# Kernel optimization log

Measured on AMD Instinct MI355X. Metric: run time of the kernel, lower is better.

Reference implementation:

```python
import jax, jax.numpy as jnp
import numpy as np

N_NODES = 100000
N_EDGES = 1600000
IN_NODE = 64
IN_EDGE = 16
HID = 128
OUT = 128
N_CONVS = 3
NEG_SLOPE = 0.01  # LeakyReLU default
LN_EPS = 1e-5


def setup_inputs() -> dict:
    key = jax.random.key(0)
    ks = jax.random.split(key, 16)
    x = jax.random.normal(ks[0], (N_NODES, IN_NODE), dtype=jnp.float32)
    edge_attr = jax.random.normal(ks[1], (N_EDGES, IN_EDGE), dtype=jnp.float32)
    edge_index = jax.random.randint(ks[2], (2, N_EDGES), 0, N_NODES, dtype=jnp.int64)
    # xavier-normal-ish init for linears
    def lin(k, fi, fo):
        return jax.random.normal(k, (fi, fo), dtype=jnp.float32) * jnp.sqrt(2.0 / (fi + fo))
    W_node = lin(ks[3], IN_NODE, HID)
    b_node = jnp.zeros((HID,), jnp.float32)
    W_edge = lin(ks[4], IN_EDGE, HID)
    b_edge = jnp.zeros((HID,), jnp.float32)
    W_conv = jax.random.normal(ks[5], (N_CONVS, HID, HID), dtype=jnp.float32) * jnp.sqrt(1.0 / HID)
    b_conv = jnp.zeros((N_CONVS, HID), jnp.float32)
    W_head = lin(ks[6], HID, OUT)
    b_head = jnp.zeros((OUT,), jnp.float32)
    ln_gamma = jnp.ones((OUT,), jnp.float32)
    ln_beta = jnp.zeros((OUT,), jnp.float32)
    return dict(x=x, edge_attr=edge_attr, edge_index=edge_index,
                W_node=W_node, b_node=b_node, W_edge=W_edge, b_edge=b_edge,
                W_conv=W_conv, b_conv=b_conv, W_head=W_head, b_head=b_head,
                ln_gamma=ln_gamma, ln_beta=ln_beta)


def _leaky_relu(x):
    return jnp.where(x >= 0, x, NEG_SLOPE * x)


def reference(x, edge_attr, edge_index, W_node, b_node, W_edge, b_edge,
              W_conv, b_conv, W_head, b_head, ln_gamma, ln_beta):
    src, dst = edge_index[0], edge_index[1]
    h = x @ W_node + b_node                  # [N, H]
    e = edge_attr @ W_edge + b_edge          # [E, H]
    skip = h
    for l in range(N_CONVS):
        # GINEConv (eps=0): nn((1+eps)*h_i + sum_j relu(h_j + e_ij)), nn = Linear + LeakyReLU
        msg = jax.nn.relu(h[src] + e)        # [E, H]
        agg = jax.ops.segment_sum(msg, dst, num_segments=N_NODES)  # [N, H]
        h = _leaky_relu((h + agg) @ W_conv[l] + b_conv[l])
    h = skip + h
    # head: Linear + LayerNorm
    y = h @ W_head + b_head                  # [N, OUT]
    mu = jnp.mean(y, axis=-1, keepdims=True)
    var = jnp.mean(jnp.square(y - mu), axis=-1, keepdims=True)
    return (y - mu) * jax.lax.rsqrt(var + LN_EPS) * ln_gamma + ln_beta
```

## Files before the change

### kernel.cpp

```cpp
#include <hip/hip_runtime.h>
#include <hip/hip_fp16.h>

constexpr int N      = 100000;
constexpr int E      = 1600000;
constexpr int F_IN   = 64;
constexpr int F_EDGE = 16;
constexpr int H      = 128;
constexpr int NB     = (N + 255) / 256;
constexpr float NEG  = 0.01f;
constexpr float EPS  = 1e-5f;

__global__ __launch_bounds__(256) void k_zero(int* __restrict__ p, int n) {
  int i = blockIdx.x * 256 + threadIdx.x;
  if (i < n) p[i] = 0;
}

__global__ __launch_bounds__(256) void k_hist(const int* __restrict__ eidx, int* __restrict__ deg) {
  int i = blockIdx.x * 256 + threadIdx.x;
  if (i < E) atomicAdd(&deg[eidx[E + i]], 1);
}

__global__ __launch_bounds__(256) void k_scan_block(const int* __restrict__ deg,
    int* __restrict__ excl, int* __restrict__ bsum) {
  __shared__ int s[256];
  int t = threadIdx.x, i = blockIdx.x * 256 + t;
  int v = (i < N) ? deg[i] : 0;
  s[t] = v; __syncthreads();
#pragma unroll
  for (int off = 1; off < 256; off <<= 1) {
    int u = (t >= off) ? s[t - off] : 0;
    __syncthreads();
    s[t] += u;
    __syncthreads();
  }
  if (i < N) excl[i] = s[t] - v;
  if (t == 255) bsum[blockIdx.x] = s[255];
}

__global__ __launch_bounds__(512) void k_scan_top(const int* __restrict__ bsum, int* __restrict__ boff) {
  __shared__ int s[512];
  int t = threadIdx.x;
  int v = (t < NB) ? bsum[t] : 0;
  s[t] = v; __syncthreads();
#pragma unroll
  for (int off = 1; off < 512; off <<= 1) {
    int u = (t >= off) ? s[t - off] : 0;
    __syncthreads();
    s[t] += u;
    __syncthreads();
  }
  if (t < NB) boff[t] = s[t] - v;
}

__global__ __launch_bounds__(256) void k_scan_add(const int* __restrict__ excl,
    const int* __restrict__ boff, int* __restrict__ rowptr, int* __restrict__ cursor) {
  int i = blockIdx.x * 256 + threadIdx.x;
  if (i < N) {
    int r = excl[i] + boff[i >> 8];
    rowptr[i] = r;
    cursor[i] = r;
  }
}

__global__ __launch_bounds__(256) void k_scatter(const int* __restrict__ eidx,
    const float* __restrict__ edge_attr, int* __restrict__ cursor,
    int* __restrict__ csr_src, uint4* __restrict__ csr_a16) {
  int i = blockIdx.x * 256 + threadIdx.x;
  if (i >= E) return;
  int d = eidx[E + i];
  int pos = atomicAdd(&cursor[d], 1);
  csr_src[pos] = eidx[i];
  const float4* ar = (const float4*)(edge_attr + (size_t)i * F_EDGE);
  float4 f0 = ar[0], f1 = ar[1], f2 = ar[2], f3 = ar[3];
  __half2 hh[8];
  hh[0] = __float22half2_rn(make_float2(f0.x, f0.y));
  hh[1] = __float22half2_rn(make_float2(f0.z, f0.w));
  hh[2] = __float22half2_rn(make_float2(f1.x, f1.y));
  hh[3] = __float22half2_rn(make_float2(f1.z, f1.w));
  hh[4] = __float22half2_rn(make_float2(f2.x, f2.y));
  hh[5] = __float22half2_rn(make_float2(f2.z, f2.w));
  hh[6] = __float22half2_rn(make_float2(f3.x, f3.y));
  hh[7] = __float22half2_rn(make_float2(f3.z, f3.w));
  const uint4* u = (const uint4*)hh;
  csr_a16[2 * (size_t)pos + 0] = u[0];
  csr_a16[2 * (size_t)pos + 1] = u[1];
}

__global__ __launch_bounds__(256) void k_node_linear(
    const float* __restrict__ x, const float* __restrict__ W,
    const float* __restrict__ b, float* __restrict__ h, __half* __restrict__ h16) {
  __shared__ float xs[8][F_IN];
  int i0 = blockIdx.x * 8;
  ((float2*)xs)[threadIdx.x] = ((const float2*)(x + (size_t)i0 * F_IN))[threadIdx.x];
  __syncthreads();
  int c = threadIdx.x & (H - 1);
  int j0 = (threadIdx.x >> 7) * 4;
  float bc = b[c];
  float acc[4] = {bc, bc, bc, bc};
#pragma unroll 8
  for (int k = 0; k < F_IN; ++k) {
    float wv = W[k * H + c];
#pragma unroll
    for (int j = 0; j < 4; ++j) acc[j] = fmaf(xs[j0 + j][k], wv, acc[j]);
  }
#pragma unroll
  for (int j = 0; j < 4; ++j) {
    size_t idx = (size_t)(i0 + j0 + j) * H + c;
    h[idx] = acc[j];
    h16[idx] = __float2half_rn(acc[j]);
  }
}

__device__ __forceinline__ float2 edge_mlp(uint4 a0, uint4 a1,
                                           const float2* __restrict__ w2, float2 t) {
  const __half2* pa = (const __half2*)&a0;
  const __half2* pb = (const __half2*)&a1;
#pragma unroll
  for (int j = 0; j < 4; ++j) {
    float2 f = __half22float2(pa[j]);
    t.x = fmaf(f.x, w2[2 * j].x, t.x);     t.y = fmaf(f.x, w2[2 * j].y, t.y);
    t.x = fmaf(f.y, w2[2 * j + 1].x, t.x); t.y = fmaf(f.y, w2[2 * j + 1].y, t.y);
  }
#pragma unroll
  for (int j = 0; j < 4; ++j) {
    float2 f = __half22float2(pb[j]);
    t.x = fmaf(f.x, w2[8 + 2 * j].x, t.x);     t.y = fmaf(f.x, w2[8 + 2 * j].y, t.y);
    t.x = fmaf(f.y, w2[8 + 2 * j + 1].x, t.x); t.y = fmaf(f.y, w2[8 + 2 * j + 1].y, t.y);
  }
  return t;
}

__global__ __launch_bounds__(256) void k_gather(
    const int* __restrict__ rowptr, const int* __restrict__ deg,
    const int* __restrict__ csr_src, const uint4* __restrict__ csr_a16,
    const __half2* __restrict__ h16, const float* __restrict__ We,
    const float* __restrict__ be, const float* __restrict__ h,
    float* __restrict__ sum) {
  int lane = threadIdx.x & 63;
  int node = (blockIdx.x * 256 + threadIdx.x) >> 6;
  if (node >= N) return;
  float2 w2[F_EDGE];
#pragma unroll
  for (int k = 0; k < F_EDGE; ++k) w2[k] = ((const float2*)(We + k * H))[lane];
  float2 bias = ((const float2*)be)[lane];
  float2 acc = ((const float2*)(h + (size_t)node * H))[lane];
  int p0 = rowptr[node];
  int pend = p0 + deg[node];
  int p = p0;
  for (; p + 2 <= pend; p += 2) {
    int s0 = csr_src[p];
    int s1 = csr_src[p + 1];
    __half2 g0 = h16[(size_t)s0 * 64 + lane];
    __half2 g1 = h16[(size_t)s1 * 64 + lane];
    uint4 a00 = csr_a16[2 * (size_t)p + 0];
    uint4 a01 = csr_a16[2 * (size_t)p + 1];
    uint4 a10 = csr_a16[2 * (size_t)p + 2];
    uint4 a11 = csr_a16[2 * (size_t)p + 3];
    float2 t0 = edge_mlp(a00, a01, w2, bias);
    float2 t1 = edge_mlp(a10, a11, w2, bias);
    float2 gf0 = __half22float2(g0);
    float2 gf1 = __half22float2(g1);
    acc.x += fmaxf(gf0.x + t0.x, 0.f) + fmaxf(gf1.x + t1.x, 0.f);
    acc.y += fmaxf(gf0.y + t0.y, 0.f) + fmaxf(gf1.y + t1.y, 0.f);
  }
  for (; p < pend; ++p) {
    int s = csr_src[p];
    __half2 g = h16[(size_t)s * 64 + lane];
    uint4 a0 = csr_a16[2 * (size_t)p + 0];
    uint4 a1 = csr_a16[2 * (size_t)p + 1];
    float2 t = edge_mlp(a0, a1, w2, bias);
    float2 gf = __half22float2(g);
    acc.x += fmaxf(gf.x + t.x, 0.f);
    acc.y += fmaxf(gf.y + t.y, 0.f);
  }
  ((float2*)sum)[(size_t)node * 64 + lane] = acc;
}

__global__ __launch_bounds__(256) void k_node_update(
    const float* __restrict__ sum, const float* __restrict__ W,
    const float* __restrict__ b, float* __restrict__ hout, __half* __restrict__ h16) {
  __shared__ float t[8][H];
  int i0 = blockIdx.x * 8;
  ((float4*)t)[threadIdx.x] = ((const float4*)(sum + (size_t)i0 * H))[threadIdx.x];
  __syncthreads();
  int c = threadIdx.x & (H - 1);
  int j0 = (threadIdx.x >> 7) * 4;
  float bc = b[c];
  float acc[4] = {bc, bc, bc, bc};
#pragma unroll 8
  for (int k = 0; k < H; ++k) {
    float wv = W[k * H + c];
#pragma unroll
    for (int j = 0; j < 4; ++j) acc[j] = fmaf(t[j0 + j][k], wv, acc[j]);
  }
#pragma unroll
  for (int j = 0; j < 4; ++j) {
    float a = acc[j];
    a = a >= 0.f ? a : NEG * a;
    size_t idx = (size_t)(i0 + j0 + j) * H + c;
    hout[idx] = a;
    h16[idx] = __float2half_rn(a);
  }
}

__global__ __launch_bounds__(128) void k_head(
    const float* __restrict__ x, const float* __restrict__ Wn,
    const float* __restrict__ bn, const float* __restrict__ hfin,
    const float* __restrict__ W, const float* __restrict__ b,
    const float* __restrict__ gamma, const float* __restrict__ beta,
    float* __restrict__ out) {
  int c = threadIdx.x;
  int i0 = blockIdx.x * 4;
  __shared__ float xs[4][F_IN];
  __shared__ float t[4][H];
  ((float2*)xs)[threadIdx.x] = ((const float2*)(x + (size_t)i0 * F_IN))[threadIdx.x];
  __syncthreads();
#pragma unroll
  for (int j = 0; j < 4; ++j) {
    float a = bn[c];
#pragma unroll 8
    for (int k = 0; k < F_IN; ++k) a = fmaf(xs[j][k], Wn[k * H + c], a);
    t[j][c] = a + hfin[(size_t)(i0 + j) * H + c];
  }
  __syncthreads();
  float bc = b[c];
  float acc[4] = {bc, bc, bc, bc};
#pragma unroll 8
  for (int k = 0; k < H; ++k) {
    float wv = W[k * H + c];
#pragma unroll
    for (int j = 0; j < 4; ++j) acc[j] = fmaf(t[j][k], wv, acc[j]);
  }
  __shared__ float ls[2][4], ls2[2][4];
  int wid = c >> 6;
#pragma unroll
  for (int j = 0; j < 4; ++j) {
    float s = acc[j], s2 = acc[j] * acc[j];
#pragma unroll
    for (int off = 32; off > 0; off >>= 1) {
      s  += __shfl_down(s, off, 64);
      s2 += __shfl_down(s2, off, 64);
    }
    if ((c & 63) == 0) { ls[wid][j] = s; ls2[wid][j] = s2; }
  }
  __syncthreads();
#pragma unroll
  for (int j = 0; j < 4; ++j) {
    float S  = ls[0][j] + ls[1][j];
    float S2 = ls2[0][j] + ls2[1][j];
    float mu  = S * (1.f / H);
    float var = S2 * (1.f / H) - mu * mu;
    float inv = rsqrtf(var + EPS);
    out[(size_t)(i0 + j) * H + c] = (acc[j] - mu) * inv * gamma[c] + beta[c];
  }
}

extern "C" void kernel_launch(void* const* d_in, const int* in_sizes, int n_in,
                              void* d_out, int out_size, void* d_ws, size_t ws_size,
                              hipStream_t stream) {
  const float* x         = (const float*)d_in[0];
  const float* edge_attr = (const float*)d_in[1];
  const int*   eidx      = (const int*)d_in[2];
  const float* W_node    = (const float*)d_in[3];
  const float* b_node    = (const float*)d_in[4];
  const float* W_edge    = (const float*)d_in[5];
  const float* b_edge    = (const float*)d_in[6];
  const float* W_conv    = (const float*)d_in[7];
  const float* b_conv    = (const float*)d_in[8];
  const float* W_head    = (const float*)d_in[9];
  const float* b_head    = (const float*)d_in[10];
  const float* gamma     = (const float*)d_in[11];
  const float* beta      = (const float*)d_in[12];
  float* out = (float*)d_out;

  size_t S = (size_t)N * H;
  float*   h       = (float*)d_ws;
  uint4*   csr_a16 = (uint4*)(h + S);
  __half*  h16     = (__half*)(csr_a16 + 2 * (size_t)E);
  int*     csr_src = (int*)(h16 + S);
  int*     deg     = csr_src + E;
  int*     excl    = deg + N;
  int*     rowptr  = excl + N;
  int*     cursor  = rowptr + N;
  int*     bsum    = cursor + N;
  int*     boff    = bsum + 512;
  float*   sum     = out;

  const int eb = (E + 255) / 256;

  k_zero<<<NB, 256, 0, stream>>>(deg, N);
  k_hist<<<eb, 256, 0, stream>>>(eidx, deg);
  k_scan_block<<<NB, 256, 0, stream>>>(deg, excl, bsum);
  k_scan_top<<<1, 512, 0, stream>>>(bsum, boff);
  k_scan_add<<<NB, 256, 0, stream>>>(excl, boff, rowptr, cursor);
  k_scatter<<<eb, 256, 0, stream>>>(eidx, edge_attr, cursor, csr_src, csr_a16);

  k_node_linear<<<N / 8, 256, 0, stream>>>(x, W_node, b_node, h, h16);

  for (int l = 0; l < 3; ++l) {
    k_gather<<<N / 4, 256, 0, stream>>>(rowptr, deg, csr_src, csr_a16,
                                        (const __half2*)h16, W_edge, b_edge, h, sum);
    k_node_update<<<N / 8, 256, 0, stream>>>(
        sum, W_conv + (size_t)l * H * H, b_conv + (size_t)l * H, h, h16);
  }

  k_head<<<N / 4, 128, 0, stream>>>(x, W_node, b_node, h, W_head, b_head, gamma, beta, out);
}
```

Before: 1.318 ms.

## Register-tile dense node kernels and use fp16 dot2 for edge MLP

Dense node kernels (node_linear, node_update, head) now process 32 or 8 nodes per block with each thread computing a 4x4 or 1x4 register tile using float4 weight loads. This cuts per-FMA weight loads and LDS traffic. In the gather kernel, the edge-feature projection is rewritten to use packed fp16 fdot2 instructions with fp16-converted edge weights, halving the FMA count. That adds some rounding error in the edge projection. The head kernel's LayerNorm reduction now works within 32-lane groups.

Result: slower. 1.365 ms (+3.6%).

```diff
diff --git a/kernel.cpp b/kernel.cpp
--- a/kernel.cpp
+++ b/kernel.cpp
@@ -9,6 +9,8 @@
 constexpr int NB     = (N + 255) / 256;
 constexpr float NEG  = 0.01f;
 constexpr float EPS  = 1e-5f;
+
+typedef _Float16 hv2 __attribute__((ext_vector_type(2)));
 
 __global__ __launch_bounds__(256) void k_zero(int* __restrict__ p, int n) {
   int i = blockIdx.x * 256 + threadIdx.x;
@@ -89,45 +91,51 @@
 __global__ __launch_bounds__(256) void k_node_linear(
     const float* __restrict__ x, const float* __restrict__ W,
     const float* __restrict__ b, float* __restrict__ h, __half* __restrict__ h16) {
-  __shared__ float xs[8][F_IN];
-  int i0 = blockIdx.x * 8;
-  ((float2*)xs)[threadIdx.x] = ((const float2*)(x + (size_t)i0 * F_IN))[threadIdx.x];
+  __shared__ float xs[32][F_IN];
+  int i0 = blockIdx.x * 32;
+  {
+    const float4* s4 = (const float4*)(x + (size_t)i0 * F_IN);
+    float4* t4 = (float4*)xs;
+#pragma unroll
+    for (int r = 0; r < 2; ++r) t4[threadIdx.x + 256 * r] = s4[threadIdx.x + 256 * r];
+  }
   __syncthreads();
-  int c = threadIdx.x & (H - 1);
-  int j0 = (threadIdx.x >> 7) * 4;
-  float bc = b[c];
-  float acc[4] = {bc, bc, bc, bc};
-#pragma unroll 8
+  int c0 = (threadIdx.x & 31) * 4;
+  int n0 = (threadIdx.x >> 5) * 4;
+  float4 bb = *(const float4*)(b + c0);
+  float4 acc[4] = {bb, bb, bb, bb};
+#pragma unroll 4
   for (int k = 0; k < F_IN; ++k) {
-    float wv = W[k * H + c];
-#pragma unroll
-    for (int j = 0; j < 4; ++j) acc[j] = fmaf(xs[j0 + j][k], wv, acc[j]);
+    float4 w4 = *(const float4*)(W + k * H + c0);
+#pragma unroll
+    for (int j = 0; j < 4; ++j) {
+      float s = xs[n0 + j][k];
+      acc[j].x = fmaf(s, w4.x, acc[j].x);
+      acc[j].y = fmaf(s, w4.y, acc[j].y);
+      acc[j].z = fmaf(s, w4.z, acc[j].z);
+      acc[j].w = fmaf(s, w4.w, acc[j].w);
+    }
   }
 #pragma unroll
   for (int j = 0; j < 4; ++j) {
-    size_t idx = (size_t)(i0 + j0 + j) * H + c;
-    h[idx] = acc[j];
-    h16[idx] = __float2half_rn(acc[j]);
-  }
-}
-
-__device__ __forceinline__ float2 edge_mlp(uint4 a0, uint4 a1,
-                                           const float2* __restrict__ w2, float2 t) {
-  const __half2* pa = (const __half2*)&a0;
-  const __half2* pb = (const __half2*)&a1;
-#pragma unroll
-  for (int j = 0; j < 4; ++j) {
-    float2 f = __half22float2(pa[j]);
-    t.x = fmaf(f.x, w2[2 * j].x, t.x);     t.y = fmaf(f.x, w2[2 * j].y, t.y);
-    t.x = fmaf(f.y, w2[2 * j + 1].x, t.x); t.y = fmaf(f.y, w2[2 * j + 1].y, t.y);
-  }
-#pragma unroll
-  for (int j = 0; j < 4; ++j) {
-    float2 f = __half22float2(pb[j]);
-    t.x = fmaf(f.x, w2[8 + 2 * j].x, t.x);     t.y = fmaf(f.x, w2[8 + 2 * j].y, t.y);
-    t.x = fmaf(f.y, w2[8 + 2 * j + 1].x, t.x); t.y = fmaf(f.y, w2[8 + 2 * j + 1].y, t.y);
-  }
-  return t;
+    size_t idx = (size_t)(i0 + n0 + j) * H + c0;
+    *(float4*)(h + idx) = acc[j];
+    __half2* ph = (__half2*)(h16 + idx);
+    ph[0] = __float22half2_rn(make_float2(acc[j].x, acc[j].y));
+    ph[1] = __float22half2_rn(make_float2(acc[j].z, acc[j].w));
+  }
+}
+
+__device__ __forceinline__ void dot16(uint4 A0, uint4 A1,
+                                      const hv2* __restrict__ wA, const hv2* __restrict__ wB,
+                                      float& tx, float& ty) {
+  unsigned u[8] = {A0.x, A0.y, A0.z, A0.w, A1.x, A1.y, A1.z, A1.w};
+#pragma unroll
+  for (int j = 0; j < 8; ++j) {
+    hv2 a = __builtin_bit_cast(hv2, u[j]);
+    tx = __builtin_amdgcn_fdot2(a, wA[j], tx, false);
+    ty = __builtin_amdgcn_fdot2(a, wB[j], ty, false);
+  }
 }
 
 __global__ __launch_bounds__(256) void k_gather(
@@ -139,9 +147,17 @@
   int lane = threadIdx.x & 63;
   int node = (blockIdx.x * 256 + threadIdx.x) >> 6;
   if (node >= N) return;
-  float2 w2[F_EDGE];
-#pragma unroll
-  for (int k = 0; k < F_EDGE; ++k) w2[k] = ((const float2*)(We + k * H))[lane];
+  int c0 = 2 * lane;
+  hv2 wA[8], wB[8];
+#pragma unroll
+  for (int j = 0; j < 8; ++j) {
+    hv2 a, bq;
+    a[0]  = (_Float16)We[(2 * j) * H + c0];
+    a[1]  = (_Float16)We[(2 * j + 1) * H + c0];
+    bq[0] = (_Float16)We[(2 * j) * H + c0 + 1];
+    bq[1] = (_Float16)We[(2 * j + 1) * H + c0 + 1];
+    wA[j] = a; wB[j] = bq;
+  }
   float2 bias = ((const float2*)be)[lane];
   float2 acc = ((const float2*)(h + (size_t)node * H))[lane];
   int p0 = rowptr[node];
@@ -152,26 +168,29 @@
     int s1 = csr_src[p + 1];
     __half2 g0 = h16[(size_t)s0 * 64 + lane];
     __half2 g1 = h16[(size_t)s1 * 64 + lane];
-    uint4 a00 = csr_a16[2 * (size_t)p + 0];
-    uint4 a01 = csr_a16[2 * (size_t)p + 1];
-    uint4 a10 = csr_a16[2 * (size_t)p + 2];
-    uint4 a11 = csr_a16[2 * (size_t)p + 3];
-    float2 t0 = edge_mlp(a00, a01, w2, bias);
-    float2 t1 = edge_mlp(a10, a11, w2, bias);
+    uint4 A0 = csr_a16[2 * (size_t)p + 0];
+    uint4 A1 = csr_a16[2 * (size_t)p + 1];
+    uint4 B0 = csr_a16[2 * (size_t)p + 2];
+    uint4 B1 = csr_a16[2 * (size_t)p + 3];
+    float t0x = bias.x, t0y = bias.y;
+    float t1x = bias.x, t1y = bias.y;
+    dot16(A0, A1, wA, wB, t0x, t0y);
+    dot16(B0, B1, wA, wB, t1x, t1y);
     float2 gf0 = __half22float2(g0);
     float2 gf1 = __half22float2(g1);
-    acc.x += fmaxf(gf0.x + t0.x, 0.f) + fmaxf(gf1.x + t1.x, 0.f);
-    acc.y += fmaxf(gf0.y + t0.y, 0.f) + fmaxf(gf1.y + t1.y, 0.f);
+    acc.x += fmaxf(gf0.x + t0x, 0.f) + fmaxf(gf1.x + t1x, 0.f);
+    acc.y += fmaxf(gf0.y + t0y, 0.f) + fmaxf(gf1.y + t1y, 0.f);
   }
   for (; p < pend; ++p) {
     int s = csr_src[p];
     __half2 g = h16[(size_t)s * 64 + lane];
-    uint4 a0 = csr_a16[2 * (size_t)p + 0];
-    uint4 a1 = csr_a16[2 * (size_t)p + 1];
-    float2 t = edge_mlp(a0, a1, w2, bias);
+    uint4 A0 = csr_a16[2 * (size_t)p + 0];
+    uint4 A1 = csr_a16[2 * (size_t)p + 1];
+    float tx = bias.x, ty = bias.y;
+    dot16(A0, A1, wA, wB, tx, ty);
     float2 gf = __half22float2(g);
-    acc.x += fmaxf(gf.x + t.x, 0.f);
-    acc.y += fmaxf(gf.y + t.y, 0.f);
+    acc.x += fmaxf(gf.x + tx, 0.f);
+    acc.y += fmaxf(gf.y + ty, 0.f);
   }
   ((float2*)sum)[(size_t)node * 64 + lane] = acc;
 }
@@ -179,80 +198,104 @@
 __global__ __launch_bounds__(256) void k_node_update(
     const float* __restrict__ sum, const float* __restrict__ W,
     const float* __restrict__ b, float* __restrict__ hout, __half* __restrict__ h16) {
-  __shared__ float t[8][H];
-  int i0 = blockIdx.x * 8;
-  ((float4*)t)[threadIdx.x] = ((const float4*)(sum + (size_t)i0 * H))[threadIdx.x];
+  __shared__ float t[32][H];
+  int i0 = blockIdx.x * 32;
+  {
+    const float4* s4 = (const float4*)(sum + (size_t)i0 * H);
+    float4* t4 = (float4*)t;
+#pragma unroll
+    for (int r = 0; r < 4; ++r) t4[threadIdx.x + 256 * r] = s4[threadIdx.x + 256 * r];
+  }
   __syncthreads();
-  int c = threadIdx.x & (H - 1);
-  int j0 = (threadIdx.x >> 7) * 4;
-  float bc = b[c];
-  float acc[4] = {bc, bc, bc, bc};
-#pragma unroll 8
+  int c0 = (threadIdx.x & 31) * 4;
+  int n0 = (threadIdx.x >> 5) * 4;
+  float4 bb = *(const float4*)(b + c0);
+  float4 acc[4] = {bb, bb, bb, bb};
+#pragma unroll 4
   for (int k = 0; k < H; ++k) {
-    float wv = W[k * H + c];
-#pragma unroll
-    for (int j = 0; j < 4; ++j) acc[j] = fmaf(t[j0 + j][k], wv, acc[j]);
+    float4 w4 = *(const float4*)(W + k * H + c0);
+#pragma unroll
+    for (int j = 0; j < 4; ++j) {
+      float s = t[n0 + j][k];
+      acc[j].x = fmaf(s, w4.x, acc[j].x);
+      acc[j].y = fmaf(s, w4.y, acc[j].y);
+      acc[j].z = fmaf(s, w4.z, acc[j].z);
+      acc[j].w = fmaf(s, w4.w, acc[j].w);
+    }
   }
 #pragma unroll
   for (int j = 0; j < 4; ++j) {
-    float a = acc[j];
-    a = a >= 0.f ? a : NEG * a;
-    size_t idx = (size_t)(i0 + j0 + j) * H + c;
-    hout[idx] = a;
-    h16[idx] = __float2half_rn(a);
-  }
-}
-
-__global__ __launch_bounds__(128) void k_head(
+    float4 a = acc[j];
+    a.x = a.x >= 0.f ? a.x : NEG * a.x;
+    a.y = a.y >= 0.f ? a.y : NEG * a.y;
+    a.z = a.z >= 0.f ? a.z : NEG * a.z;
+    a.w = a.w >= 0.f ? a.w : NEG * a.w;
+    size_t idx = (size_t)(i0 + n0 + j) * H + c0;
+    *(float4*)(hout + idx) = a;
+    __half2* ph = (__half2*)(h16 + idx);
+    ph[0] = __float22half2_rn(make_float2(a.x, a.y));
+    ph[1] = __float22half2_rn(make_float2(a.z, a.w));
+  }
+}
+
+__global__ __launch_bounds__(256) void k_head(
     const float* __restrict__ x, const float* __restrict__ Wn,
     const float* __restrict__ bn, const float* __restrict__ hfin,
     const float* __restrict__ W, const float* __restrict__ b,
     const float* __restrict__ gamma, const float* __restrict__ beta,
     float* __restrict__ out) {
-  int c = threadIdx.x;
-  int i0 = blockIdx.x * 4;
-  __shared__ float xs[4][F_IN];
-  __shared__ float t[4][H];
-  ((float2*)xs)[threadIdx.x] = ((const float2*)(x + (size_t)i0 * F_IN))[threadIdx.x];
+  __shared__ float xs[8][F_IN];
+  __shared__ float t[8][H];
+  int i0 = blockIdx.x * 8;
+  if (threadIdx.x < 128)
+    ((float4*)xs)[threadIdx.x] = ((const float4*)(x + (size_t)i0 * F_IN))[threadIdx.x];
   __syncthreads();
-#pragma unroll
-  for (int j = 0; j < 4; ++j) {
-    float a = bn[c];
-#pragma unroll 8
-    for (int k = 0; k < F_IN; ++k) a = fmaf(xs[j][k], Wn[k * H + c], a);
-    t[j][c] = a + hfin[(size_t)(i0 + j) * H + c];
-  }
+  int c0 = (threadIdx.x & 31) * 4;
+  int ng = threadIdx.x >> 5;
+  float4 sk = *(const float4*)(bn + c0);
+#pragma unroll 4
+  for (int k = 0; k < F_IN; ++k) {
+    float4 w4 = *(const float4*)(Wn + k * H + c0);
+    float s = xs[ng][k];
+    sk.x = fmaf(s, w4.x, sk.x);
+    sk.y = fmaf(s, w4.y, sk.y);
+    sk.z = fmaf(s, w4.z, sk.z);
+    sk.w = fmaf(s, w4.w, sk.w);
+  }
+  float4 hf = *(const float4*)(hfin + (size_t)(i0 + ng) * H + c0);
+  sk.x += hf.x; sk.y += hf.y; sk.z += hf.z; sk.w += hf.w;
+  *(float4*)&t[ng][c0] = sk;
   __syncthreads();
-  float bc = b[c];
-  float acc[4] = {bc, bc, bc, bc};
-#pragma unroll 8
+  float4 acc = *(const float4*)(b + c0);
+#pragma unroll 4
   for (int k = 0; k < H; ++k) {
-    float wv = W[k * H + c];
-#pragma unroll
-    for (int j = 0; j < 4; ++j) acc[j] = fmaf(t[j][k], wv, acc[j]);
-  }
-  __shared__ float ls[2][4], ls2[2][4];
-  int wid = c >> 6;
-#pragma unroll
-  for (int j = 0; j < 4; ++j) {
-    float s = acc[j], s2 = acc[j] * acc[j];
-#pragma unroll
-    for (int off = 32; off > 0; off >>= 1) {
-      s  += __shfl_down(s, off, 64);
-      s2 += __shfl_down(s2, off, 64);
-    }
-    if ((c & 63) == 0) { ls[wid][j] = s; ls2[wid][j] = s2; }
-  }
-  __syncthreads();
-#pragma unroll
-  for (int j = 0; j < 4; ++j) {
-    float S  = ls[0][j] + ls[1][j];
-    float S2 = ls2[0][j] + ls2[1][j];
-    float mu  = S * (1.f / H);
-    float var = S2 * (1.f / H) - mu * mu;
-    float inv = rsqrtf(var + EPS);
-    out[(size_t)(i0 + j) * H + c] = (acc[j] - mu) * inv * gamma[c] + beta[c];
-  }
+    float4 w4 = *(const float4*)(W + k * H + c0);
+    float s = t[ng][k];
+    acc.x = fmaf(s, w4.x, acc.x);
+    acc.y = fmaf(s, w4.y, acc.y);
+    acc.z = fmaf(s, w4.z, acc.z);
+    acc.w = fmaf(s, w4.w, acc.w);
+  }
+  float S  = acc.x + acc.y + acc.z + acc.w;
+  float S2 = acc.x * acc.x + acc.y * acc.y + acc.z * acc.z + acc.w * acc.w;
+#pragma unroll
+  for (int off = 16; off > 0; off >>= 1) {
+    S  += __shfl_down(S, off, 32);
+    S2 += __shfl_down(S2, off, 32);
+  }
+  S  = __shfl(S, 0, 32);
+  S2 = __shfl(S2, 0, 32);
+  float mu  = S * (1.f / H);
+  float var = S2 * (1.f / H) - mu * mu;
+  float inv = rsqrtf(var + EPS);
+  float4 g4 = *(const float4*)(gamma + c0);
+  float4 b4 = *(const float4*)(beta + c0);
+  float4 o;
+  o.x = (acc.x - mu) * inv * g4.x + b4.x;
+  o.y = (acc.y - mu) * inv * g4.y + b4.y;
+  o.z = (acc.z - mu) * inv * g4.z + b4.z;
+  o.w = (acc.w - mu) * inv * g4.w + b4.w;
+  *(float4*)(out + (size_t)(i0 + ng) * H + c0) = o;
 }
 
 extern "C" void kernel_launch(void* const* d_in, const int* in_sizes, int n_in,
@@ -295,14 +338,14 @@
   k_scan_add<<<NB, 256, 0, stream>>>(excl, boff, rowptr, cursor);
   k_scatter<<<eb, 256, 0, stream>>>(eidx, edge_attr, cursor, csr_src, csr_a16);
 
-  k_node_linear<<<N / 8, 256, 0, stream>>>(x, W_node, b_node, h, h16);
+  k_node_linear<<<N / 32, 256, 0, stream>>>(x, W_node, b_node, h, h16);
 
   for (int l = 0; l < 3; ++l) {
     k_gather<<<N / 4, 256, 0, stream>>>(rowptr, deg, csr_src, csr_a16,
                                         (const __half2*)h16, W_edge, b_edge, h, sum);
-    k_node_update<<<N / 8, 256, 0, stream>>>(
+    k_node_update<<<N / 32, 256, 0, stream>>>(
         sum, W_conv + (size_t)l * H * H, b_conv + (size_t)l * H, h, h16);
   }
 
-  k_head<<<N / 4, 128, 0, stream>>>(x, W_node, b_node, h, W_head, b_head, gamma, beta, out);
-}
+  k_head<<<N / 8, 256, 0, stream>>>(x, W_node, b_node, h, W_head, b_head, gamma, beta, out);
+}
```
